# Performance work log

Measured on AMD Instinct MI355X. Metric: run time of the kernel, lower is better.

Reference implementation:

```python
import jax, jax.numpy as jnp
import numpy as np

B, DIM_IN, T = 16, 512, 2048
DIM_OUT2 = 512 * 2  # dim_out * 2 (GLU halves it)
K = 3
STYLE = 128
SCALE_CONV = 1.0 / np.sqrt(DIM_IN * K ** 2).astype(np.float32)  # fan_in = dim_in * k^2 (as in source)
SCALE_LIN = 1.0 / np.sqrt(STYLE).astype(np.float32)


def setup_inputs() -> dict:
    key = jax.random.key(0)
    ks = jax.random.split(key, 6)
    x = jax.random.normal(ks[0], (B, DIM_IN, T), dtype=jnp.float32)
    c_src = jax.random.normal(ks[1], (B, STYLE), dtype=jnp.float32)
    c_trg = jax.random.normal(ks[2], (B, STYLE), dtype=jnp.float32)
    # EqualLinear params (lr_mul=1): weight ~ N(0,1), bias filled with bias_init=1
    w_s = jax.random.normal(ks[3], (DIM_IN, STYLE), dtype=jnp.float32)
    b_s = jnp.ones((DIM_IN,), dtype=jnp.float32)
    w_b = jax.random.normal(ks[4], (DIM_IN, STYLE), dtype=jnp.float32)
    b_b = jnp.ones((DIM_IN,), dtype=jnp.float32)
    weight = jax.random.normal(ks[5], (1, DIM_OUT2, DIM_IN, K), dtype=jnp.float32)
    return {"x": x, "c_src": c_src, "c_trg": c_trg,
            "w_s": w_s, "b_s": b_s, "w_b": w_b, "b_b": b_b, "weight": weight}


def reference(x, c_src, c_trg, w_s, b_s, w_b, b_b, weight):
    bsz, cin, t = x.shape
    cout = weight.shape[1]  # dim_out * 2
    k = weight.shape[3]
    # EqualLinear: F.linear(c, w*scale, bias)
    s = (c_trg @ (w_s * SCALE_LIN).T + b_s).reshape(bsz, 1, cin, 1)
    beta = (c_trg @ (w_b * SCALE_LIN).T + b_b).reshape(bsz, 1, cin, 1)
    w = SCALE_CONV * (weight * s + beta)               # [B, Cout, Cin, K]
    demod = jax.lax.rsqrt(jnp.sum(w * w, axis=(2, 3)) + 1e-8)   # [B, Cout]
    demod_mean = jnp.mean(w.reshape(bsz, cout, -1), axis=2)      # [B, Cout]
    w = (w - demod_mean[:, :, None, None]) * demod[:, :, None, None]
    # batch-as-groups conv1d
    w = w.reshape(bsz * cout, cin, k)
    xr = x.reshape(1, bsz * cin, t)
    out = jax.lax.conv_general_dilated(
        xr, w, window_strides=(1,), padding=[(k // 2, k // 2)],
        dimension_numbers=("NCH", "OIH", "NCH"), feature_group_count=bsz)
    out = out.reshape(bsz, cout, -1)
    a, g = jnp.split(out, 2, axis=1)  # GLU on channel dim
    return a * jax.nn.sigmoid(g)
```

## Files before the change

### kernel.cpp

```cpp
#include <hip/hip_runtime.h>
#include <math.h>

typedef __attribute__((ext_vector_type(8))) short short8;
typedef __attribute__((ext_vector_type(4))) float f32x4;
typedef unsigned short ushortT;

#define NB     16
#define CIN    512
#define TT     2048
#define COUT2  1024
#define NSTYLE 128
#define KKTOT  1536
#define TPAD   2050
#define NKT    24

#define SCALE_LIN  0.088388347648318447f
#define SCALE_CONV 0.014731391274719736f

__device__ __forceinline__ ushortT f2bf(float f) {
  union { float f; unsigned u; } v; v.f = f;
  unsigned r = v.u + 0x7fffu + ((v.u >> 16) & 1u);
  return (ushortT)(r >> 16);
}

__device__ __forceinline__ void gload16(const void* g, void* l) {
  __builtin_amdgcn_global_load_lds(
      (const __attribute__((address_space(1))) void*)g,
      (__attribute__((address_space(3))) void*)l, 16, 0, 0);
}

__global__ void style_kernel(const float* __restrict__ c_trg,
                             const float* __restrict__ w_s, const float* __restrict__ b_s,
                             const float* __restrict__ w_b, const float* __restrict__ b_b,
                             float* __restrict__ s, float* __restrict__ beta,
                             ushortT* __restrict__ xT) {
  int gid = blockIdx.x * 256 + threadIdx.x;
  int b = gid >> 9, ci = gid & 511;
  const float* ct = c_trg + b * NSTYLE;
  const float* ws = w_s + ci * NSTYLE;
  const float* wb = w_b + ci * NSTYLE;
  float as = 0.f, ab = 0.f;
#pragma unroll 8
  for (int j = 0; j < NSTYLE; ++j) {
    float c = ct[j];
    as += c * ws[j];
    ab += c * wb[j];
  }
  s[gid]    = as * SCALE_LIN + b_s[ci];
  beta[gid] = ab * SCALE_LIN + b_b[ci];
  xT[(size_t)b * TPAD * CIN + ci] = 0;
  xT[((size_t)b * TPAD + TPAD - 1) * CIN + ci] = 0;
}

__global__ void xpose_kernel(const float* __restrict__ x, ushortT* __restrict__ xT) {
  int b = blockIdx.z, ct = blockIdx.y, tt = blockIdx.x;
  int t0 = tt * 64, ci0 = ct * 64;
  __shared__ float tile[64][65];
  const float* xB = x + (size_t)b * CIN * TT;
  int rr = threadIdx.x >> 4;
  int c4 = threadIdx.x & 15;
#pragma unroll
  for (int it = 0; it < 4; ++it) {
    int ci = rr + it * 16;
    float4 v = *(const float4*)(xB + (size_t)(ci0 + ci) * TT + t0 + c4 * 4);
    tile[ci][c4 * 4 + 0] = v.x; tile[ci][c4 * 4 + 1] = v.y;
    tile[ci][c4 * 4 + 2] = v.z; tile[ci][c4 * 4 + 3] = v.w;
  }
  __syncthreads();
  ushortT* xTB = xT + (size_t)b * TPAD * CIN;
#pragma unroll
  for (int it = 0; it < 4; ++it) {
    int t = rr + it * 16;
    ushort4 o;
    o.x = f2bf(tile[c4 * 4 + 0][t]); o.y = f2bf(tile[c4 * 4 + 1][t]);
    o.z = f2bf(tile[c4 * 4 + 2][t]); o.w = f2bf(tile[c4 * 4 + 3][t]);
    *(ushort4*)(xTB + (size_t)(1 + t0 + t) * CIN + ci0 + c4 * 4) = o;
  }
}

__global__ void modw_kernel(const float* __restrict__ weight,
                            const float* __restrict__ s, const float* __restrict__ beta,
                            ushortT* __restrict__ wnorm) {
  int co = blockIdx.x, b = blockIdx.y, tid = threadIdx.x;
  int ci = tid * 2;
  const float* wp = weight + (size_t)co * CIN * 3 + (size_t)ci * 3;
  float s0 = s[b * CIN + ci],     s1 = s[b * CIN + ci + 1];
  float e0 = beta[b * CIN + ci],  e1 = beta[b * CIN + ci + 1];
  float w0 = SCALE_CONV * (wp[0] * s0 + e0);
  float w1 = SCALE_CONV * (wp[1] * s0 + e0);
  float w2 = SCALE_CONV * (wp[2] * s0 + e0);
  float w3 = SCALE_CONV * (wp[3] * s1 + e1);
  float w4 = SCALE_CONV * (wp[4] * s1 + e1);
  float w5 = SCALE_CONV * (wp[5] * s1 + e1);
  float sum = w0 + w1 + w2 + w3 + w4 + w5;
  float sq  = w0*w0 + w1*w1 + w2*w2 + w3*w3 + w4*w4 + w5*w5;
#pragma unroll
  for (int off = 32; off; off >>= 1) {
    sum += __shfl_xor(sum, off);
    sq  += __shfl_xor(sq,  off);
  }
  __shared__ float rs[4], rq[4];
  if ((tid & 63) == 0) { rs[tid >> 6] = sum; rq[tid >> 6] = sq; }
  __syncthreads();
  float tsum = rs[0] + rs[1] + rs[2] + rs[3];
  float tsq  = rq[0] + rq[1] + rq[2] + rq[3];
  float mean  = tsum * (1.0f / 1536.0f);
  float demod = rsqrtf(tsq + 1e-8f);
  int r = ((co & 511) << 1) | (co >> 9);
  ushortT* dst = wnorm + ((size_t)b * COUT2 + r) * KKTOT;
  ushort2 p0, p1, p2;
  p0.x = f2bf((w0 - mean) * demod); p0.y = f2bf((w3 - mean) * demod);
  p1.x = f2bf((w1 - mean) * demod); p1.y = f2bf((w4 - mean) * demod);
  p2.x = f2bf((w2 - mean) * demod); p2.y = f2bf((w5 - mean) * demod);
  *(ushort2*)(dst +        ci) = p0;
  *(ushort2*)(dst +  512 + ci) = p1;
  *(ushort2*)(dst + 1024 + ci) = p2;
}


#define AFRAG(d, s, f) (*(const short8*)(ldsc + ((d) * 4 + (s)) * 16384 + aoff + (f) * 1024))
#define BFRAG(d, s, g) (*(const short8*)(ldsc + ((d) * 4 + 2 + (s)) * 16384 + boff + (g) * 1024))

#define STAGE_A(d, s, kt) do {                                                   \
    int kc_ = (kt) * 64 + (s) * 32;                                              \
    gload16(wB + (size_t)(co0 + r0) * KKTOT + kc_ + jbs8,                        \
            ldsw + ((d) * 4 + (s)) * 8192 + tid * 8);                            \
    gload16(wB + (size_t)(co0 + r0 + 128) * KKTOT + kc_ + jbs8,                  \
            ldsw + ((d) * 4 + (s)) * 8192 + 4096 + tid * 8);                     \
  } while (0)

#define STAGE_B(d, s, kt) do {                                                   \
    int kc_ = (kt) * 64 + (s) * 32;                                              \
    int tap_ = kc_ >> 9; int ci_ = kc_ & 511;                                    \
    gload16(xB + (size_t)(t0 + r0 + tap_) * CIN + ci_ + jbs8,                    \
            ldsw + ((d) * 4 + 2 + (s)) * 8192 + tid * 8);                        \
    gload16(xB + (size_t)(t0 + r0 + 128 + tap_) * CIN + ci_ + jbs8,              \
            ldsw + ((d) * 4 + 2 + (s)) * 8192 + 4096 + tid * 8);                 \
  } while (0)

#define PHASE(d, s, mh, STAGES, VMN) do {                                        \
    short8 a0 = AFRAG(d, s, (mh) * 4 + 0);                                       \
    short8 a1 = AFRAG(d, s, (mh) * 4 + 1);                                       \
    short8 a2 = AFRAG(d, s, (mh) * 4 + 2);                                       \
    short8 a3 = AFRAG(d, s, (mh) * 4 + 3);                                       \
    if ((mh) == 0) {                                                             \
      bf0 = BFRAG(d, s, 0); bf1 = BFRAG(d, s, 1);                                \
      bf2 = BFRAG(d, s, 2); bf3 = BFRAG(d, s, 3);                                \
    }                                                                            \
    STAGES;                                                                      \
    if ((VMN) == 6)      asm volatile("s_waitcnt vmcnt(6)" ::: "memory");        \
    else if ((VMN) == 0) asm volatile("s_waitcnt vmcnt(0)" ::: "memory");        \
    __builtin_amdgcn_sched_barrier(0);                                           \
    __builtin_amdgcn_s_barrier();                                                \
    __builtin_amdgcn_sched_barrier(0);                                           \
    __builtin_amdgcn_s_setprio(1);                                               \
    acc[(mh)*4+0][0] = __builtin_amdgcn_mfma_f32_16x16x32_bf16(a0, bf0, acc[(mh)*4+0][0], 0, 0, 0); \
    acc[(mh)*4+0][1] = __builtin_amdgcn_mfma_f32_16x16x32_bf16(a0, bf1, acc[(mh)*4+0][1], 0, 0, 0); \
    acc[(mh)*4+0][2] = __builtin_amdgcn_mfma_f32_16x16x32_bf16(a0, bf2, acc[(mh)*4+0][2], 0, 0, 0); \
    acc[(mh)*4+0][3] = __builtin_amdgcn_mfma_f32_16x16x32_bf16(a0, bf3, acc[(mh)*4+0][3], 0, 0, 0); \
    acc[(mh)*4+1][0] = __builtin_amdgcn_mfma_f32_16x16x32_bf16(a1, bf0, acc[(mh)*4+1][0], 0, 0, 0); \
    acc[(mh)*4+1][1] = __builtin_amdgcn_mfma_f32_16x16x32_bf16(a1, bf1, acc[(mh)*4+1][1], 0, 0, 0); \
    acc[(mh)*4+1][2] = __builtin_amdgcn_mfma_f32_16x16x32_bf16(a1, bf2, acc[(mh)*4+1][2], 0, 0, 0); \
    acc[(mh)*4+1][3] = __builtin_amdgcn_mfma_f32_16x16x32_bf16(a1, bf3, acc[(mh)*4+1][3], 0, 0, 0); \
    acc[(mh)*4+2][0] = __builtin_amdgcn_mfma_f32_16x16x32_bf16(a2, bf0, acc[(mh)*4+2][0], 0, 0, 0); \
    acc[(mh)*4+2][1] = __builtin_amdgcn_mfma_f32_16x16x32_bf16(a2, bf1, acc[(mh)*4+2][1], 0, 0, 0); \
    acc[(mh)*4+2][2] = __builtin_amdgcn_mfma_f32_16x16x32_bf16(a2, bf2, acc[(mh)*4+2][2], 0, 0, 0); \
    acc[(mh)*4+2][3] = __builtin_amdgcn_mfma_f32_16x16x32_bf16(a2, bf3, acc[(mh)*4+2][3], 0, 0, 0); \
    acc[(mh)*4+3][0] = __builtin_amdgcn_mfma_f32_16x16x32_bf16(a3, bf0, acc[(mh)*4+3][0], 0, 0, 0); \
    acc[(mh)*4+3][1] = __builtin_amdgcn_mfma_f32_16x16x32_bf16(a3, bf1, acc[(mh)*4+3][1], 0, 0, 0); \
    acc[(mh)*4+3][2] = __builtin_amdgcn_mfma_f32_16x16x32_bf16(a3, bf2, acc[(mh)*4+3][2], 0, 0, 0); \
    acc[(mh)*4+3][3] = __builtin_amdgcn_mfma_f32_16x16x32_bf16(a3, bf3, acc[(mh)*4+3][3], 0, 0, 0); \
    __builtin_amdgcn_s_setprio(0);                                               \
    __builtin_amdgcn_sched_barrier(0);                                           \
    __builtin_amdgcn_s_barrier();                                                \
    __builtin_amdgcn_sched_barrier(0);                                           \
  } while (0)

__global__ __launch_bounds__(512, 2)
void conv_gemm8(const ushortT* __restrict__ wnorm, const ushortT* __restrict__ xT,
                float* __restrict__ out) {
  extern __shared__ ushortT ldsw[];
  const char* ldsc = (const char*)ldsw;

  int orig = blockIdx.x;
  int wgid = (orig & 7) * 64 + (orig >> 3);
  int b  = wgid >> 5;
  int i5 = wgid & 31;
  int mp = i5 >> 4, r2 = i5 & 15;
  int nt = r2 >> 1, mt = mp * 2 + (r2 & 1);
  int co0 = mt * 256, t0 = nt * 256;

  int tid = threadIdx.x;
  int l = tid & 63, w = tid >> 6;
  int wm = w & 1, wn = w >> 1;

  int r0 = tid >> 2;
  int jbs8 = (((tid & 3) ^ ((r0 >> 1) & 3)) << 3);
  int cb = ((l >> 4) ^ ((l >> 1) & 3));
  int aoff = (wm * 128 + (l & 15)) * 64 + cb * 16;
  int boff = (wn * 64  + (l & 15)) * 64 + cb * 16;

  const ushortT* wB = wnorm + (size_t)b * COUT2 * KKTOT;
  const ushortT* xB = xT + (size_t)b * TPAD * CIN;

  f32x4 acc[8][4];
#pragma unroll
  for (int i = 0; i < 8; ++i)
#pragma unroll
    for (int j = 0; j < 4; ++j)
      acc[i][j] = (f32x4){0.f, 0.f, 0.f, 0.f};
  short8 bf0 = {}, bf1 = {}, bf2 = {}, bf3 = {};

  STAGE_A(0, 0, 0); STAGE_B(0, 0, 0); STAGE_A(0, 1, 0); STAGE_B(0, 1, 0);
  STAGE_B(1, 0, 1); STAGE_A(1, 0, 1); STAGE_B(1, 1, 1);
  asm volatile("s_waitcnt vmcnt(6)" ::: "memory");
  __builtin_amdgcn_sched_barrier(0);
  __builtin_amdgcn_s_barrier();
  __builtin_amdgcn_sched_barrier(0);

  for (int j = 0; j < 11; ++j) {
    int kt1 = 2 * j + 1;
    int ktn0 = 2 * j + 2, ktn1 = 2 * j + 3;
    PHASE(0, 0, 0, STAGE_A(1, 1, kt1),  -1);
    PHASE(0, 0, 1, STAGE_B(0, 0, ktn0), -1);
    PHASE(0, 1, 0, STAGE_A(0, 0, ktn0), -1);
    PHASE(0, 1, 1, STAGE_B(0, 1, ktn0),  6);
    PHASE(1, 0, 0, STAGE_A(0, 1, ktn0), -1);
    PHASE(1, 0, 1, STAGE_B(1, 0, ktn1), -1);
    PHASE(1, 1, 0, STAGE_A(1, 0, ktn1), -1);
    PHASE(1, 1, 1, STAGE_B(1, 1, ktn1),  6);
  }
  PHASE(0, 0, 0, STAGE_A(1, 1, 23), -1);
  PHASE(0, 0, 1, {}, -1);
  PHASE(0, 1, 0, {}, -1);
  PHASE(0, 1, 1, {},  0);
  PHASE(1, 0, 0, {}, -1);
  PHASE(1, 0, 1, {}, -1);
  PHASE(1, 1, 0, {}, -1);
  PHASE(1, 1, 1, {}, -1);

#pragma unroll
  for (int f = 0; f < 8; ++f) {
    int cop = co0 + wm * 128 + f * 16 + ((l >> 4) << 2);
    int c = cop >> 1;
    size_t obase = ((size_t)b * (COUT2 / 2) + c) * TT;
#pragma unroll
    for (int g = 0; g < 4; ++g) {
      int t = t0 + wn * 64 + g * 16 + (l & 15);
      f32x4 v = acc[f][g];
      out[obase + t]      = v.x / (1.f + __expf(-v.y));
      out[obase + TT + t] = v.z / (1.f + __expf(-v.w));
    }
  }
}

extern "C" void kernel_launch(void* const* d_in, const int* in_sizes, int n_in,
                              void* d_out, int out_size, void* d_ws, size_t ws_size,
                              hipStream_t stream) {
  const float* x      = (const float*)d_in[0];
  const float* c_trg  = (const float*)d_in[2];
  const float* w_s    = (const float*)d_in[3];
  const float* b_s    = (const float*)d_in[4];
  const float* w_b    = (const float*)d_in[5];
  const float* b_b    = (const float*)d_in[6];
  const float* weight = (const float*)d_in[7];
  float* out = (float*)d_out;

  char* ws = (char*)d_ws;
  float*   s     = (float*)ws;
  float*   beta  = (float*)(ws + 32768);
  ushortT* xT    = (ushortT*)(ws + 65536);
  ushortT* wnorm = (ushortT*)(ws + 65536 + 33587200);

  hipFuncSetAttribute((const void*)conv_gemm8,
                      hipFuncAttributeMaxDynamicSharedMemorySize, 131072);

  style_kernel<<<32, 256, 0, stream>>>(c_trg, w_s, b_s, w_b, b_b, s, beta, xT);
  xpose_kernel<<<dim3(32, 8, 16), 256, 0, stream>>>(x, xT);
  modw_kernel<<<dim3(1024, 16), 256, 0, stream>>>(weight, s, beta, wnorm);
  conv_gemm8<<<512, 512, 131072, stream>>>(wnorm, xT, out);
}
```

Baseline: 136.8 us.

## Loop batches inside modw kernel and relax GEMM scheduling barriers

```diff
diff --git a/kernel.cpp b/kernel.cpp
--- a/kernel.cpp
+++ b/kernel.cpp
@@ -81,40 +81,45 @@
 __global__ void modw_kernel(const float* __restrict__ weight,
                             const float* __restrict__ s, const float* __restrict__ beta,
                             ushortT* __restrict__ wnorm) {
-  int co = blockIdx.x, b = blockIdx.y, tid = threadIdx.x;
+  int co = blockIdx.x, tid = threadIdx.x;
   int ci = tid * 2;
-  const float* wp = weight + (size_t)co * CIN * 3 + (size_t)ci * 3;
-  float s0 = s[b * CIN + ci],     s1 = s[b * CIN + ci + 1];
-  float e0 = beta[b * CIN + ci],  e1 = beta[b * CIN + ci + 1];
-  float w0 = SCALE_CONV * (wp[0] * s0 + e0);
-  float w1 = SCALE_CONV * (wp[1] * s0 + e0);
-  float w2 = SCALE_CONV * (wp[2] * s0 + e0);
-  float w3 = SCALE_CONV * (wp[3] * s1 + e1);
-  float w4 = SCALE_CONV * (wp[4] * s1 + e1);
-  float w5 = SCALE_CONV * (wp[5] * s1 + e1);
-  float sum = w0 + w1 + w2 + w3 + w4 + w5;
-  float sq  = w0*w0 + w1*w1 + w2*w2 + w3*w3 + w4*w4 + w5*w5;
-#pragma unroll
-  for (int off = 32; off; off >>= 1) {
-    sum += __shfl_xor(sum, off);
-    sq  += __shfl_xor(sq,  off);
-  }
+  const float* wp = weight + (size_t)co * KKTOT + (size_t)ci * 3;
+  float2 va = *(const float2*)(wp);
+  float2 vb = *(const float2*)(wp + 2);
+  float2 vc = *(const float2*)(wp + 4);
+  float v0 = va.x, v1 = va.y, v2 = vb.x, v3 = vb.y, v4 = vc.x, v5 = vc.y;
+  int r = ((co & 511) << 1) | (co >> 9);
   __shared__ float rs[4], rq[4];
-  if ((tid & 63) == 0) { rs[tid >> 6] = sum; rq[tid >> 6] = sq; }
-  __syncthreads();
-  float tsum = rs[0] + rs[1] + rs[2] + rs[3];
-  float tsq  = rq[0] + rq[1] + rq[2] + rq[3];
-  float mean  = tsum * (1.0f / 1536.0f);
-  float demod = rsqrtf(tsq + 1e-8f);
-  int r = ((co & 511) << 1) | (co >> 9);
-  ushortT* dst = wnorm + ((size_t)b * COUT2 + r) * KKTOT;
-  ushort2 p0, p1, p2;
-  p0.x = f2bf((w0 - mean) * demod); p0.y = f2bf((w3 - mean) * demod);
-  p1.x = f2bf((w1 - mean) * demod); p1.y = f2bf((w4 - mean) * demod);
-  p2.x = f2bf((w2 - mean) * demod); p2.y = f2bf((w5 - mean) * demod);
-  *(ushort2*)(dst +        ci) = p0;
-  *(ushort2*)(dst +  512 + ci) = p1;
-  *(ushort2*)(dst + 1024 + ci) = p2;
+  for (int b = 0; b < NB; ++b) {
+    float2 sv = *(const float2*)(s + b * CIN + ci);
+    float2 ev = *(const float2*)(beta + b * CIN + ci);
+    float w0 = SCALE_CONV * (v0 * sv.x + ev.x);
+    float w1 = SCALE_CONV * (v1 * sv.x + ev.x);
+    float w2 = SCALE_CONV * (v2 * sv.x + ev.x);
+    float w3 = SCALE_CONV * (v3 * sv.y + ev.y);
+    float w4 = SCALE_CONV * (v4 * sv.y + ev.y);
+    float w5 = SCALE_CONV * (v5 * sv.y + ev.y);
+    float sum = w0 + w1 + w2 + w3 + w4 + w5;
+    float sq  = w0*w0 + w1*w1 + w2*w2 + w3*w3 + w4*w4 + w5*w5;
+#pragma unroll
+    for (int off = 32; off; off >>= 1) {
+      sum += __shfl_xor(sum, off);
+      sq  += __shfl_xor(sq,  off);
+    }
+    if ((tid & 63) == 0) { rs[tid >> 6] = sum; rq[tid >> 6] = sq; }
+    __syncthreads();
+    float mean  = (rs[0] + rs[1] + rs[2] + rs[3]) * (1.0f / 1536.0f);
+    float demod = rsqrtf(rq[0] + rq[1] + rq[2] + rq[3] + 1e-8f);
+    ushortT* dst = wnorm + ((size_t)b * COUT2 + r) * KKTOT;
+    ushort2 p0, p1, p2;
+    p0.x = f2bf((w0 - mean) * demod); p0.y = f2bf((w3 - mean) * demod);
+    p1.x = f2bf((w1 - mean) * demod); p1.y = f2bf((w4 - mean) * demod);
+    p2.x = f2bf((w2 - mean) * demod); p2.y = f2bf((w5 - mean) * demod);
+    *(ushort2*)(dst +        ci) = p0;
+    *(ushort2*)(dst +  512 + ci) = p1;
+    *(ushort2*)(dst + 1024 + ci) = p2;
+    __syncthreads();
+  }
 }
 
 
@@ -150,9 +155,8 @@
     STAGES;                                                                      \
     if ((VMN) == 6)      asm volatile("s_waitcnt vmcnt(6)" ::: "memory");        \
     else if ((VMN) == 0) asm volatile("s_waitcnt vmcnt(0)" ::: "memory");        \
-    __builtin_amdgcn_sched_barrier(0);                                           \
     __builtin_amdgcn_s_barrier();                                                \
-    __builtin_amdgcn_sched_barrier(0);                                           \
+    asm volatile("s_waitcnt lgkmcnt(0)" ::: "memory");                           \
     __builtin_amdgcn_s_setprio(1);                                               \
     acc[(mh)*4+0][0] = __builtin_amdgcn_mfma_f32_16x16x32_bf16(a0, bf0, acc[(mh)*4+0][0], 0, 0, 0); \
     acc[(mh)*4+0][1] = __builtin_amdgcn_mfma_f32_16x16x32_bf16(a0, bf1, acc[(mh)*4+0][1], 0, 0, 0); \
@@ -171,9 +175,7 @@
     acc[(mh)*4+3][2] = __builtin_amdgcn_mfma_f32_16x16x32_bf16(a3, bf2, acc[(mh)*4+3][2], 0, 0, 0); \
     acc[(mh)*4+3][3] = __builtin_amdgcn_mfma_f32_16x16x32_bf16(a3, bf3, acc[(mh)*4+3][3], 0, 0, 0); \
     __builtin_amdgcn_s_setprio(0);                                               \
-    __builtin_amdgcn_sched_barrier(0);                                           \
     __builtin_amdgcn_s_barrier();                                                \
-    __builtin_amdgcn_sched_barrier(0);                                           \
   } while (0)
 
 __global__ __launch_bounds__(512, 2)
@@ -214,9 +216,7 @@
   STAGE_A(0, 0, 0); STAGE_B(0, 0, 0); STAGE_A(0, 1, 0); STAGE_B(0, 1, 0);
   STAGE_B(1, 0, 1); STAGE_A(1, 0, 1); STAGE_B(1, 1, 1);
   asm volatile("s_waitcnt vmcnt(6)" ::: "memory");
-  __builtin_amdgcn_sched_barrier(0);
   __builtin_amdgcn_s_barrier();
-  __builtin_amdgcn_sched_barrier(0);
 
   for (int j = 0; j < 11; ++j) {
     int kt1 = 2 * j + 1;
@@ -277,6 +277,6 @@
 
   style_kernel<<<32, 256, 0, stream>>>(c_trg, w_s, b_s, w_b, b_b, s, beta, xT);
   xpose_kernel<<<dim3(32, 8, 16), 256, 0, stream>>>(x, xT);
-  modw_kernel<<<dim3(1024, 16), 256, 0, stream>>>(weight, s, beta, wnorm);
+  modw_kernel<<<1024, 256, 0, stream>>>(weight, s, beta, wnorm);
   conv_gemm8<<<512, 512, 131072, stream>>>(wnorm, xT, out);
 }
```

Result: slower. 140.0 us (+2.3%).
